# Kernel optimization log

Measured on AMD Instinct MI355X. Metric: run time of the kernel, lower is better.

Reference implementation:

```python
import jax, jax.numpy as jnp
import numpy as np

N_NODES = 100000
N_EDGES = 1600000
IN_FEATS = 128
HIDDEN = 256
NUM_CLASSES = 1


def setup_inputs() -> dict:
    key = jax.random.key(0)
    ks = jax.random.split(key, 6)
    x = jax.random.normal(ks[0], (N_NODES, IN_FEATS), dtype=jnp.float32)
    src = jax.random.randint(ks[1], (N_EDGES,), 0, N_NODES, dtype=jnp.int64 if jax.config.jax_enable_x64 else jnp.int32).astype(jnp.int32)
    dst = jax.random.randint(ks[2], (N_EDGES,), 0, N_NODES, dtype=jnp.int32)
    W1 = jax.random.normal(ks[3], (IN_FEATS, HIDDEN), dtype=jnp.float32) * (1.0 / np.sqrt(IN_FEATS))
    b1 = jnp.zeros((HIDDEN,), dtype=jnp.float32)
    W2 = jax.random.normal(ks[4], (HIDDEN, NUM_CLASSES), dtype=jnp.float32) * (1.0 / np.sqrt(HIDDEN))
    b2 = jnp.zeros((NUM_CLASSES,), dtype=jnp.float32)
    return {"x": x, "src": src, "dst": dst, "W1": W1, "b1": b1, "W2": W2, "b2": b2}


def _graph_conv(x, src, dst, W, b):
    """DGL GraphConv with norm='both': D_out^{-1/2} gather -> scatter-add -> D_in^{-1/2}, then XW+b."""
    n = x.shape[0]
    ones = jnp.ones(src.shape[0], dtype=x.dtype)
    deg_out = jax.ops.segment_sum(ones, src, num_segments=n)
    deg_in = jax.ops.segment_sum(ones, dst, num_segments=n)
    norm_out = jax.lax.rsqrt(jnp.maximum(deg_out, 1.0))  # [N]
    norm_in = jax.lax.rsqrt(jnp.maximum(deg_in, 1.0))    # [N]
    h = x * norm_out[:, None]                 # [N, F]
    msg = h[src]                              # [E, F] gather (memory-bound)
    agg = jax.ops.segment_sum(msg, dst, num_segments=n)  # [N, F] scatter-add
    agg = agg * norm_in[:, None]
    return agg @ W + b


def reference(x, src, dst, W1, b1, W2, b2):
    # layer 0: GraphConv -> relu (dropout p=0.0 -> identity)
    h = jax.nn.relu(_graph_conv(x, src, dst, W1, b1))
    # output layer: GraphConv -> sigmoid
    h = jax.nn.sigmoid(_graph_conv(h, src, dst, W2, b2))
    return h
```

## Files before the change

kernel.cpp:

```cpp
#include <hip/hip_runtime.h>
#include <math.h>

#define NN 100000
#define NE 1600000
#define INF 128
#define HID 256
#define SCAN_BLK 256
#define NSCAN ((NN + SCAN_BLK - 1) / SCAN_BLK)
#define FGRP 8
#define FRNG (NN / FGRP)
#define NC 32
#define CHUNK (NE / NC)
#define HRNG 25000
#define MIDF (FGRP * NC)
#define MIDX 256
#define MIDW 5

typedef short bf16x8 __attribute__((ext_vector_type(8)));
typedef float f32x4 __attribute__((ext_vector_type(4)));

__device__ __forceinline__ unsigned int f2bf(float f) {
    unsigned int u = __float_as_uint(f);
    u = u + 0x7FFFu + ((u >> 16) & 1u);
    return u >> 16;
}

__launch_bounds__(1024)
__global__ void k_hist(const int* __restrict__ src, const int* __restrict__ dst,
                       unsigned int* __restrict__ hop, unsigned int* __restrict__ hip) {
    __shared__ unsigned int h[HRNG / 2];
    const int type = blockIdx.x & 1;
    const int gp = (blockIdx.x >> 1) & 3;
    const int c = blockIdx.x >> 3;
    const int lo = gp * HRNG;
    for (int i = threadIdx.x; i < HRNG / 2; i += 1024) h[i] = 0;
    __syncthreads();
    const int4* a4 = reinterpret_cast<const int4*>((type ? dst : src) + c * CHUNK);
    for (int k = threadIdx.x; k < CHUNK / 4; k += 1024) {
        int4 v = a4[k];
        int i0 = v.x - lo, i1 = v.y - lo, i2 = v.z - lo, i3 = v.w - lo;
        if ((unsigned)i0 < HRNG) atomicAdd(&h[i0 >> 1], 1u << ((i0 & 1) << 4));
        if ((unsigned)i1 < HRNG) atomicAdd(&h[i1 >> 1], 1u << ((i1 & 1) << 4));
        if ((unsigned)i2 < HRNG) atomicAdd(&h[i2 >> 1], 1u << ((i2 & 1) << 4));
        if ((unsigned)i3 < HRNG) atomicAdd(&h[i3 >> 1], 1u << ((i3 & 1) << 4));
    }
    __syncthreads();
    unsigned int* o = (type ? hip : hop) + (size_t)c * (NN / 2) + gp * (HRNG / 2);
    for (int i = threadIdx.x; i < HRNG / 2; i += 1024) o[i] = h[i];
}

__global__ void k_norms2(const unsigned int* __restrict__ hop, const unsigned int* __restrict__ hip,
                         float* __restrict__ nrm_out, float* __restrict__ nrm_in,
                         int* __restrict__ deg_in, int* __restrict__ partial) {
    __shared__ int sh[SCAN_BLK];
    int v = blockIdx.x * SCAN_BLK + threadIdx.x;
    int so = 0, si = 0;
    if (v < NN) {
        int w = v >> 1, sft = (v & 1) << 4;
        #pragma unroll
        for (int c = 0; c < NC; ++c) {
            so += (hop[(size_t)c * (NN / 2) + w] >> sft) & 0xFFFFu;
            si += (hip[(size_t)c * (NN / 2) + w] >> sft) & 0xFFFFu;
        }
        nrm_out[v] = rsqrtf(fmaxf((float)so, 1.0f));
        nrm_in[v]  = rsqrtf(fmaxf((float)si, 1.0f));
        deg_in[v]  = si;
    }
    sh[threadIdx.x] = si;
    __syncthreads();
    for (int off = SCAN_BLK / 2; off > 0; off >>= 1) {
        if (threadIdx.x < off) sh[threadIdx.x] += sh[threadIdx.x + off];
        __syncthreads();
    }
    if (threadIdx.x == 0) partial[blockIdx.x] = sh[0];
}

__global__ void k_scan2(int* __restrict__ partial) {
    int lane = threadIdx.x;
    int carry = 0;
    for (int c = 0; c < NSCAN; c += 64) {
        int idx = c + lane;
        int v = (idx < NSCAN) ? partial[idx] : 0;
        int s = v;
        #pragma unroll
        for (int off = 1; off < 64; off <<= 1) {
            int t = __shfl_up(s, off, 64);
            if (lane >= off) s += t;
        }
        if (idx < NSCAN) partial[idx] = s - v + carry;
        carry += __shfl(s, 63, 64);
    }
}

__global__ void k_scan3c(const int* __restrict__ deg_in, const int* __restrict__ partial,
                         int* __restrict__ offsets, const unsigned int* __restrict__ hip,
                         int* __restrict__ cbase) {
    __shared__ int sh[SCAN_BLK];
    int i = blockIdx.x * SCAN_BLK + threadIdx.x;
    int v = (i < NN) ? deg_in[i] : 0;
    sh[threadIdx.x] = v;
    __syncthreads();
    for (int off = 1; off < SCAN_BLK; off <<= 1) {
        int t = (threadIdx.x >= off) ? sh[threadIdx.x - off] : 0;
        __syncthreads();
        sh[threadIdx.x] += t;
        __syncthreads();
    }
    int ex = sh[threadIdx.x] - v + partial[blockIdx.x];
    if (i < NN) {
        offsets[i] = ex;
        int run = ex;
        int w = i >> 1, sft = (i & 1) << 4;
        #pragma unroll
        for (int c = 0; c < NC; ++c) {
            cbase[(size_t)c * NN + i] = run;
            run += (hip[(size_t)c * (NN / 2) + w] >> sft) & 0xFFFFu;
        }
    }
    if (i == 0) offsets[NN] = NE;
}

__launch_bounds__(1024)
__global__ void k_mid(const int* __restrict__ src, const int* __restrict__ dst,
                      const int* __restrict__ cbase, int* __restrict__ csr_src,
                      const float* __restrict__ x, const float* __restrict__ nrm_out,
                      unsigned int* __restrict__ xs,
                      const float* __restrict__ W1, const float* __restrict__ b1,
                      const float* __restrict__ W2, unsigned short* __restrict__ fragW,
                      float2* __restrict__ bw) {
    __shared__ int cur[FRNG];
    const int bid = blockIdx.x;
    if (bid < MIDF) {
        const int g = bid & (FGRP - 1);
        const int c = bid >> 3;
        const int lo = g * FRNG;
        const int* cb = cbase + (size_t)c * NN + lo;
        for (int i = threadIdx.x; i < FRNG; i += 1024) cur[i] = cb[i];
        __syncthreads();
        const int e0 = c * CHUNK;
        const int4* d4 = reinterpret_cast<const int4*>(dst + e0);
        for (int k = threadIdx.x; k < CHUNK / 4; k += 1024) {
            int4 v = d4[k];
            int e = e0 + k * 4;
            int i0 = v.x - lo, i1 = v.y - lo, i2 = v.z - lo, i3 = v.w - lo;
            if ((unsigned)i0 < FRNG) { int p = atomicAdd(&cur[i0], 1); csr_src[p] = src[e]; }
            if ((unsigned)i1 < FRNG) { int p = atomicAdd(&cur[i1], 1); csr_src[p] = src[e + 1]; }
            if ((unsigned)i2 < FRNG) { int p = atomicAdd(&cur[i2], 1); csr_src[p] = src[e + 2]; }
            if ((unsigned)i3 < FRNG) { int p = atomicAdd(&cur[i3], 1); csr_src[p] = src[e + 3]; }
        }
    } else if (bid < MIDF + MIDX) {
        const int nU2 = NN * (INF / 4);
        for (int i = (bid - MIDF) * 1024 + threadIdx.x; i < nU2; i += MIDX * 1024) {
            int row = i >> 5;
            float n = nrm_out[row];
            float4 v = *reinterpret_cast<const float4*>(x + (size_t)i * 4);
            uint2 r;
            r.x = f2bf(v.x * n) | (f2bf(v.y * n) << 16);
            r.y = f2bf(v.z * n) | (f2bf(v.w * n) << 16);
            *reinterpret_cast<uint2*>(xs + (size_t)i * 2) = r;
        }
    } else {
        int idx = (bid - MIDF - MIDX) * 1024 + threadIdx.x;
        if (idx < 4096) {
            int l = idx & 63, ks = (idx >> 6) & 3, nt = idx >> 8;
            int kbase = ks * 32 + ((l >> 4) << 3);
            int col = nt * 16 + (l & 15);
            bf16x8 r;
            #pragma unroll
            for (int i = 0; i < 8; ++i)
                r[i] = (short)f2bf(W1[(size_t)(kbase + i) * HID + col]);
            *reinterpret_cast<bf16x8*>(fragW + (size_t)idx * 8) = r;
        } else if (idx < 4096 + HID) {
            int n = idx - 4096;
            bw[n] = make_float2(b1[n], W2[n]);
        }
    }
}

__global__ void k_gather(const unsigned int* __restrict__ xs, const int* __restrict__ offsets,
                         const int* __restrict__ csr_src, const float* __restrict__ nrm_in,
                         unsigned int* __restrict__ aggb) {
    int row = blockIdx.x * 4 + (threadIdx.x >> 6);
    if (row >= NN) return;
    int lane = threadIdx.x & 63;
    int beg = offsets[row], end = offsets[row + 1];
    float alo[8], ahi[8];
    #pragma unroll
    for (int q = 0; q < 8; ++q) { alo[q] = 0.f; ahi[q] = 0.f; }
    int j = beg;
    if (j + 8 <= end) {
        int s[8];
        #pragma unroll
        for (int q = 0; q < 8; ++q) s[q] = csr_src[j + q];
        while (true) {
            unsigned int p[8];
            #pragma unroll
            for (int q = 0; q < 8; ++q) p[q] = xs[(size_t)s[q] * 64 + lane];
            j += 8;
            bool more = (j + 8 <= end);
            if (more) {
                #pragma unroll
                for (int q = 0; q < 8; ++q) s[q] = csr_src[j + q];
            }
            #pragma unroll
            for (int q = 0; q < 8; ++q) {
                alo[q] += __uint_as_float(p[q] << 16);
                ahi[q] += __uint_as_float(p[q] & 0xFFFF0000u);
            }
            if (!more) break;
        }
    }
    for (; j < end; ++j) {
        unsigned int p0 = xs[(size_t)csr_src[j] * 64 + lane];
        alo[0] += __uint_as_float(p0 << 16);
        ahi[0] += __uint_as_float(p0 & 0xFFFF0000u);
    }
    float ni = nrm_in[row];
    float lo = (((alo[0] + alo[1]) + (alo[2] + alo[3])) +
                ((alo[4] + alo[5]) + (alo[6] + alo[7]))) * ni;
    float hi = (((ahi[0] + ahi[1]) + (ahi[2] + ahi[3])) +
                ((ahi[4] + ahi[5]) + (ahi[6] + ahi[7]))) * ni;
    aggb[(size_t)row * 64 + lane] = f2bf(lo) | (f2bf(hi) << 16);
}

__launch_bounds__(256)
__global__ void k_gemm(const unsigned short* __restrict__ aggb,
                       const unsigned short* __restrict__ fragW,
                       const float2* __restrict__ bw, const float* __restrict__ nrm_out,
                       float* __restrict__ z) {
    const int l = threadIdx.x & 63;
    const int w = threadIdx.x >> 6;
    const int r0 = blockIdx.x * 64 + w * 16;
    const int n15 = l & 15;
    const int hi = l >> 4;
    const int arow = r0 + n15;

    bf16x8 a[4];
    if (arow < NN) {
        #pragma unroll
        for (int ks = 0; ks < 4; ++ks)
            a[ks] = *reinterpret_cast<const bf16x8*>(aggb + (size_t)arow * INF + ks * 32 + (hi << 3));
    } else {
        #pragma unroll
        for (int ks = 0; ks < 4; ++ks) a[ks] = (bf16x8){0, 0, 0, 0, 0, 0, 0, 0};
    }

    float pacc[4] = {0.f, 0.f, 0.f, 0.f};
    #pragma unroll
    for (int nt = 0; nt < 16; ++nt) {
        f32x4 acc = {0.f, 0.f, 0.f, 0.f};
        #pragma unroll
        for (int ks = 0; ks < 4; ++ks) {
            bf16x8 b = *reinterpret_cast<const bf16x8*>(fragW + (size_t)(((nt * 4 + ks) * 64 + l) << 3));
            acc = __builtin_amdgcn_mfma_f32_16x16x32_bf16(a[ks], b, acc, 0, 0, 0);
        }
        float2 c = bw[nt * 16 + n15];
        #pragma unroll
        for (int g = 0; g < 4; ++g)
            pacc[g] += fmaxf(acc[g] + c.x, 0.f) * c.y;
    }
    #pragma unroll
    for (int off = 1; off < 16; off <<= 1) {
        #pragma unroll
        for (int g = 0; g < 4; ++g) pacc[g] += __shfl_xor(pacc[g], off, 64);
    }
    if (n15 == 0) {
        #pragma unroll
        for (int g = 0; g < 4; ++g) {
            int gr = r0 + (hi << 2) + g;
            if (gr < NN) z[gr] = nrm_out[gr] * pacc[g];
        }
    }
}

__global__ void k_out(const float* __restrict__ z, const int* __restrict__ offsets,
                      const int* __restrict__ csr_src, const float* __restrict__ nrm_in,
                      const float* __restrict__ b2, float* __restrict__ out) {
    int v = blockIdx.x * 16 + (threadIdx.x >> 4);
    if (v >= NN) return;
    int li = threadIdx.x & 15;
    int beg = offsets[v], end = offsets[v + 1];
    float s = 0.f;
    for (int j = beg + li; j < end; j += 16) s += z[csr_src[j]];
    #pragma unroll
    for (int off = 1; off < 16; off <<= 1) s += __shfl_xor(s, off, 64);
    if (li == 0) {
        float val = s * nrm_in[v] + b2[0];
        out[v] = 1.0f / (1.0f + expf(-val));
    }
}

extern "C" void kernel_launch(void* const* d_in, const int* in_sizes, int n_in,
                              void* d_out, int out_size, void* d_ws, size_t ws_size,
                              hipStream_t stream) {
    const float* x   = (const float*)d_in[0];
    const int*   src = (const int*)d_in[1];
    const int*   dst = (const int*)d_in[2];
    const float* W1  = (const float*)d_in[3];
    const float* b1  = (const float*)d_in[4];
    const float* W2  = (const float*)d_in[5];
    const float* b2  = (const float*)d_in[6];
    float* out = (float*)d_out;

    int*   deg_in  = (int*)d_ws;
    int*   offsets = deg_in + NN;
    int*   partial = offsets + NN + 1;
    int*   csr_src = partial + NSCAN;
    float* nrm_out = (float*)(csr_src + NE);
    float* nrm_in  = nrm_out + NN;
    float* z       = nrm_in + NN;
    float2* bw     = (float2*)(z + NN);
    unsigned int* xs   = (unsigned int*)(bw + HID);
    unsigned int* aggb = xs + (size_t)NN * 64;
    unsigned short* fragW = (unsigned short*)(aggb + (size_t)NN * 64);
    unsigned int* hop = xs;
    unsigned int* hip = hop + (size_t)NC * (NN / 2);
    int* cbase = (int*)aggb;

    k_hist<<<2 * 4 * NC, 1024, 0, stream>>>(src, dst, hop, hip);
    k_norms2<<<NSCAN, SCAN_BLK, 0, stream>>>(hop, hip, nrm_out, nrm_in, deg_in, partial);
    k_scan2<<<1, 64, 0, stream>>>(partial);
    k_scan3c<<<NSCAN, SCAN_BLK, 0, stream>>>(deg_in, partial, offsets, hip, cbase);
    k_mid<<<MIDF + MIDX + MIDW, 1024, 0, stream>>>(src, dst, cbase, csr_src,
                                                   x, nrm_out, xs, W1, b1, W2, fragW, bw);
    k_gather<<<NN / 4, 256, 0, stream>>>(xs, offsets, csr_src, nrm_in, aggb);
    k_gemm<<<(NN + 63) / 64, 256, 0, stream>>>((const unsigned short*)aggb, fragW, bw, nrm_out, z);
    k_out<<<(NN + 15) / 16, 256, 0, stream>>>(z, offsets, csr_src, nrm_in, b2, out);
}
```

Before: 197.2 us.

## Fuse neighbor gather into MFMA GEMM kernel via shared-memory tile

```diff
diff --git a/kernel.cpp b/kernel.cpp
--- a/kernel.cpp
+++ b/kernel.cpp
@@ -177,72 +177,65 @@
     }
 }
 
-__global__ void k_gather(const unsigned int* __restrict__ xs, const int* __restrict__ offsets,
-                         const int* __restrict__ csr_src, const float* __restrict__ nrm_in,
-                         unsigned int* __restrict__ aggb) {
-    int row = blockIdx.x * 4 + (threadIdx.x >> 6);
-    if (row >= NN) return;
-    int lane = threadIdx.x & 63;
-    int beg = offsets[row], end = offsets[row + 1];
-    float alo[8], ahi[8];
-    #pragma unroll
-    for (int q = 0; q < 8; ++q) { alo[q] = 0.f; ahi[q] = 0.f; }
-    int j = beg;
-    if (j + 8 <= end) {
-        int s[8];
-        #pragma unroll
-        for (int q = 0; q < 8; ++q) s[q] = csr_src[j + q];
-        while (true) {
-            unsigned int p[8];
-            #pragma unroll
-            for (int q = 0; q < 8; ++q) p[q] = xs[(size_t)s[q] * 64 + lane];
-            j += 8;
-            bool more = (j + 8 <= end);
-            if (more) {
-                #pragma unroll
-                for (int q = 0; q < 8; ++q) s[q] = csr_src[j + q];
-            }
-            #pragma unroll
-            for (int q = 0; q < 8; ++q) {
-                alo[q] += __uint_as_float(p[q] << 16);
-                ahi[q] += __uint_as_float(p[q] & 0xFFFF0000u);
-            }
-            if (!more) break;
-        }
-    }
-    for (; j < end; ++j) {
-        unsigned int p0 = xs[(size_t)csr_src[j] * 64 + lane];
-        alo[0] += __uint_as_float(p0 << 16);
-        ahi[0] += __uint_as_float(p0 & 0xFFFF0000u);
-    }
-    float ni = nrm_in[row];
-    float lo = (((alo[0] + alo[1]) + (alo[2] + alo[3])) +
-                ((alo[4] + alo[5]) + (alo[6] + alo[7]))) * ni;
-    float hi = (((ahi[0] + ahi[1]) + (ahi[2] + ahi[3])) +
-                ((ahi[4] + ahi[5]) + (ahi[6] + ahi[7]))) * ni;
-    aggb[(size_t)row * 64 + lane] = f2bf(lo) | (f2bf(hi) << 16);
-}
-
 __launch_bounds__(256)
-__global__ void k_gemm(const unsigned short* __restrict__ aggb,
-                       const unsigned short* __restrict__ fragW,
-                       const float2* __restrict__ bw, const float* __restrict__ nrm_out,
-                       float* __restrict__ z) {
+__global__ void k_gg(const unsigned int* __restrict__ xs, const int* __restrict__ offsets,
+                     const int* __restrict__ csr_src, const float* __restrict__ nrm_in,
+                     const unsigned short* __restrict__ fragW, const float2* __restrict__ bw,
+                     const float* __restrict__ nrm_out, float* __restrict__ z) {
+    __shared__ __align__(16) unsigned int tile[4][16][68];
     const int l = threadIdx.x & 63;
     const int w = threadIdx.x >> 6;
     const int r0 = blockIdx.x * 64 + w * 16;
+
+    for (int rr = 0; rr < 16; ++rr) {
+        int row = r0 + rr;
+        unsigned int packed = 0;
+        if (row < NN) {
+            int beg = offsets[row], end = offsets[row + 1];
+            float a0 = 0.f, a1 = 0.f, b0 = 0.f, b1 = 0.f;
+            float c0 = 0.f, c1 = 0.f, d0 = 0.f, d1 = 0.f;
+            int j = beg;
+            if (j + 4 <= end) {
+                int s0 = csr_src[j], s1 = csr_src[j + 1], s2 = csr_src[j + 2], s3 = csr_src[j + 3];
+                while (true) {
+                    unsigned int p0 = xs[(size_t)s0 * 64 + l];
+                    unsigned int p1 = xs[(size_t)s1 * 64 + l];
+                    unsigned int p2 = xs[(size_t)s2 * 64 + l];
+                    unsigned int p3 = xs[(size_t)s3 * 64 + l];
+                    j += 4;
+                    bool more = (j + 4 <= end);
+                    if (more) {
+                        s0 = csr_src[j]; s1 = csr_src[j + 1];
+                        s2 = csr_src[j + 2]; s3 = csr_src[j + 3];
+                    }
+                    a0 += __uint_as_float(p0 << 16); a1 += __uint_as_float(p0 & 0xFFFF0000u);
+                    b0 += __uint_as_float(p1 << 16); b1 += __uint_as_float(p1 & 0xFFFF0000u);
+                    c0 += __uint_as_float(p2 << 16); c1 += __uint_as_float(p2 & 0xFFFF0000u);
+                    d0 += __uint_as_float(p3 << 16); d1 += __uint_as_float(p3 & 0xFFFF0000u);
+                    if (!more) break;
+                }
+            }
+            for (; j < end; ++j) {
+                unsigned int p0 = xs[(size_t)csr_src[j] * 64 + l];
+                a0 += __uint_as_float(p0 << 16);
+                a1 += __uint_as_float(p0 & 0xFFFF0000u);
+            }
+            float ni = nrm_in[row];
+            float lo = ((a0 + b0) + (c0 + d0)) * ni;
+            float hi2 = ((a1 + b1) + (c1 + d1)) * ni;
+            packed = f2bf(lo) | (f2bf(hi2) << 16);
+        }
+        tile[w][rr][l] = packed;
+    }
+    __syncthreads();
+
     const int n15 = l & 15;
     const int hi = l >> 4;
-    const int arow = r0 + n15;
-
     bf16x8 a[4];
-    if (arow < NN) {
-        #pragma unroll
-        for (int ks = 0; ks < 4; ++ks)
-            a[ks] = *reinterpret_cast<const bf16x8*>(aggb + (size_t)arow * INF + ks * 32 + (hi << 3));
-    } else {
-        #pragma unroll
-        for (int ks = 0; ks < 4; ++ks) a[ks] = (bf16x8){0, 0, 0, 0, 0, 0, 0, 0};
+    #pragma unroll
+    for (int ks = 0; ks < 4; ++ks) {
+        uint4 u = *reinterpret_cast<const uint4*>(&tile[w][n15][ks * 16 + hi * 4]);
+        a[ks] = *reinterpret_cast<bf16x8*>(&u);
     }
 
     float pacc[4] = {0.f, 0.f, 0.f, 0.f};
@@ -311,11 +304,11 @@
     float* z       = nrm_in + NN;
     float2* bw     = (float2*)(z + NN);
     unsigned int* xs   = (unsigned int*)(bw + HID);
-    unsigned int* aggb = xs + (size_t)NN * 64;
-    unsigned short* fragW = (unsigned short*)(aggb + (size_t)NN * 64);
+    unsigned int* scr2 = xs + (size_t)NN * 64;
+    unsigned short* fragW = (unsigned short*)(scr2 + (size_t)NN * 64);
     unsigned int* hop = xs;
     unsigned int* hip = hop + (size_t)NC * (NN / 2);
-    int* cbase = (int*)aggb;
+    int* cbase = (int*)scr2;
 
     k_hist<<<2 * 4 * NC, 1024, 0, stream>>>(src, dst, hop, hip);
     k_norms2<<<NSCAN, SCAN_BLK, 0, stream>>>(hop, hip, nrm_out, nrm_in, deg_in, partial);
@@ -323,7 +316,7 @@
     k_scan3c<<<NSCAN, SCAN_BLK, 0, stream>>>(deg_in, partial, offsets, hip, cbase);
     k_mid<<<MIDF + MIDX + MIDW, 1024, 0, stream>>>(src, dst, cbase, csr_src,
                                                    x, nrm_out, xs, W1, b1, W2, fragW, bw);
-    k_gather<<<NN / 4, 256, 0, stream>>>(xs, offsets, csr_src, nrm_in, aggb);
-    k_gemm<<<(NN + 63) / 64, 256, 0, stream>>>((const unsigned short*)aggb, fragW, bw, nrm_out, z);
+    k_gg<<<(NN + 63) / 64, 256, 0, stream>>>(xs, offsets, csr_src, nrm_in,
+                                             fragW, bw, nrm_out, z);
     k_out<<<(NN + 15) / 16, 256, 0, stream>>>(z, offsets, csr_src, nrm_in, b2, out);
 }
```

Measured after the change: 259.6 us. 31.6% more time.
